# Performance work log

Hardware: AMD Instinct MI355X
Metric: run time of the kernel (lower is better)

Reference implementation:

```python
import jax, jax.numpy as jnp
import numpy as np

N_NODES = 50000
N_EDGES = 800000
IN_DIM = 64
HEADS = 8
DHEAD = 8
CLAMP = 5.0


def _xavier(key, shape, fan_in, fan_out):
    std = jnp.sqrt(2.0 / (fan_in + fan_out))
    return std * jax.random.normal(key, shape, dtype=jnp.float32)


def setup_inputs() -> dict:
    key = jax.random.key(0)
    ks = jax.random.split(key, 12)
    HD = HEADS * DHEAD
    x = jax.random.normal(ks[0], (N_NODES, IN_DIM), dtype=jnp.float32)
    edge_attr = jax.random.normal(ks[1], (N_EDGES, IN_DIM), dtype=jnp.float32)
    edge_index = jax.random.randint(ks[2], (2, N_EDGES), 0, N_NODES, dtype=jnp.int32)
    # Linear weights stored as [in, out] so y = x @ W + b
    WQ = _xavier(ks[3], (IN_DIM, HD), IN_DIM, HD)
    bQ = jnp.zeros((HD,), jnp.float32)
    WK = _xavier(ks[4], (IN_DIM, HD), IN_DIM, HD)
    bK = jnp.zeros((HD,), jnp.float32)
    WE = _xavier(ks[5], (IN_DIM, 2 * HD), IN_DIM, 2 * HD)
    bE = jnp.zeros((2 * HD,), jnp.float32)
    WV = _xavier(ks[6], (IN_DIM, HD), IN_DIM, HD)
    bV = jnp.zeros((HD,), jnp.float32)
    Aw = _xavier(ks[7], (DHEAD, HEADS, 1), DHEAD * HEADS, 1)
    VeRow = _xavier(ks[8], (DHEAD, HEADS, DHEAD), DHEAD * HEADS, DHEAD)
    return {"x": x, "edge_attr": edge_attr, "edge_index": edge_index,
            "WQ": WQ, "bQ": bQ, "WK": WK, "bK": bK, "WE": WE, "bE": bE,
            "WV": WV, "bV": bV, "Aw": Aw, "VeRow": VeRow}


def _forward(x, edge_attr, edge_index, WQ, bQ, WK, bK, WE, bE, WV, bV, Aw, VeRow):
    N = x.shape[0]
    src_idx = edge_index[0]
    dst_idx = edge_index[1]
    Q_h = (x @ WQ + bQ).reshape(N, HEADS, DHEAD)
    K_h = (x @ WK + bK).reshape(N, HEADS, DHEAD)
    V_h = (x @ WV + bV).reshape(N, HEADS, DHEAD)
    E = (edge_attr @ WE + bE).reshape(-1, HEADS, 2 * DHEAD)  # [E,H,2D]
    E_w, E_b = E[:, :, :DHEAD], E[:, :, DHEAD:]
    # per-edge score: gather + signed-sqrt transform
    score = K_h[src_idx] + Q_h[dst_idx]              # [E,H,D]
    score = score * E_w
    score = jnp.sqrt(jax.nn.relu(score)) - jnp.sqrt(jax.nn.relu(-score))
    score = score + E_b                               # act = Identity
    e_t = score
    wE = score.reshape(score.shape[0], HEADS * DHEAD)
    # attention logits: contract over head dim with Aw -> [E,H,1]
    logit = jnp.einsum('ehd,dhc->ehc', score, Aw)
    logit = jnp.clip(logit, -CLAMP, CLAMP)
    # segment softmax over destination nodes (pyg_softmax)
    smax = jax.ops.segment_max(logit, dst_idx, num_segments=N)
    ex = jnp.exp(logit - smax[dst_idx])
    denom = jax.ops.segment_sum(ex, dst_idx, num_segments=N)[dst_idx] + 1e-16
    attn = ex / denom                                 # [E,H,1], dropout p=0
    # message passing: scatter-add weighted values
    msg = V_h[src_idx] * attn                         # [E,H,D]
    wV = jax.ops.segment_sum(msg, dst_idx, num_segments=N)
    # edge enhancement
    rowV = jax.ops.segment_sum(e_t * attn, dst_idx, num_segments=N)  # [N,H,D]
    wV = wV + jnp.einsum('nhd,dhc->nhc', rowV, VeRow)
    return wV, wE


def reference(x, edge_attr, edge_index, WQ, bQ, WK, bK, WE, bE, WV, bV, Aw, VeRow):
    return _forward(x, edge_attr, edge_index, WQ, bQ, WK, bK, WE, bE, WV, bV, Aw, VeRow)
```

## Files before the change

### kernel.cpp

```cpp
#include <hip/hip_runtime.h>
#include <hip/hip_bf16.h>
#include <math.h>

#define N_NODES 50000
#define N_EDGES 800000
#define CLAMP_V 5.0f

typedef short short8 __attribute__((ext_vector_type(8)));
typedef float f32x4  __attribute__((ext_vector_type(4)));

static __device__ inline short f2bf(float x) {
    __hip_bfloat16 h = __float2bfloat16(x);
    return __builtin_bit_cast(short, h);
}
static __device__ inline float bf2f(short s) {
    unsigned u = ((unsigned)(unsigned short)s) << 16;
    return __builtin_bit_cast(float, u);
}

__global__ __launch_bounds__(256) void qkv_kernel(
    const float* __restrict__ x,
    const float* __restrict__ WQ, const float* __restrict__ bQ,
    const float* __restrict__ WK, const float* __restrict__ bK,
    const float* __restrict__ WV, const float* __restrict__ bV,
    float* __restrict__ Q, float* __restrict__ K, float* __restrict__ V)
{
    const int t = threadIdx.x;
    const int c = t & 63;
    const int nl = t >> 6;
    const int base = blockIdx.x * 16;

    float accQ[4], accK[4], accV[4];
    int nodes[4];
#pragma unroll
    for (int j = 0; j < 4; ++j) {
        nodes[j] = base + j * 4 + nl;
        accQ[j] = bQ[c]; accK[j] = bK[c]; accV[j] = bV[c];
    }
    for (int k = 0; k < 64; ++k) {
        const float wq = WQ[k * 64 + c];
        const float wk = WK[k * 64 + c];
        const float wv = WV[k * 64 + c];
#pragma unroll
        for (int j = 0; j < 4; ++j) {
            const float xv = x[nodes[j] * 64 + k];
            accQ[j] += xv * wq;
            accK[j] += xv * wk;
            accV[j] += xv * wv;
        }
    }
#pragma unroll
    for (int j = 0; j < 4; ++j) {
        const int n = nodes[j];
        Q[n * 64 + c] = accQ[j];
        K[n * 64 + c] = accK[j];
        V[n * 64 + c] = accV[j];
    }
}

__global__ __launch_bounds__(256, 3) void edge_kernel(
    const float* __restrict__ edge_attr,
    const int* __restrict__ src_idx, const int* __restrict__ dst_idx,
    const float* __restrict__ WE, const float* __restrict__ bE,
    const float* __restrict__ Aw,
    const float* __restrict__ Qn, const float* __restrict__ Kn,
    const float* __restrict__ Vn, const float* __restrict__ VeRow,
    float* __restrict__ wE_out, float* __restrict__ denom,
    float* __restrict__ wV_num)
{
    __shared__ __align__(16) char raw[41984];
    __shared__ float bEs[128];

    short8* Bhi = (short8*)raw;
    short8* Blo = (short8*)(raw + 16384);

    const int t = threadIdx.x;
    const int wave = t >> 6;
    const int lane = t & 63;

    short* BhiE = (short*)raw;
    short* BloE = (short*)(raw + 16384);
    for (int i = t; i < 8192; i += 256) {
        const int j  = i & 7;
        const int ln = (i >> 3) & 63;
        const int kh = (i >> 9) & 1;
        const int ct = i >> 10;
        const int k   = kh * 32 + ((ln >> 4) << 3) + j;
        const int col = (ct << 4) + (ln & 15);
        const float w = WE[k * 128 + col];
        const short hb = f2bf(w);
        BhiE[i] = hb;
        BloE[i] = f2bf(w - bf2f(hb));
    }
    if (t < 128) bEs[t] = bE[t];
    __syncthreads();

    float* Ebuf_w = (float*)(raw + 32768 + wave * 2304);

    const int h    = lane >> 3;
    const int kk   = lane & 7;
    const int g    = lane >> 4;
    const int c4   = lane & 15;
    const int h16k = (h << 4) + kk;
    const int ewoff = (h16k + (h16k >> 3)) << 2;
    const int eboff = ((h16k + 8) + ((h16k + 8) >> 3)) << 2;

    const float aw = Aw[kk * 8 + h];
    float veR[8];
#pragma unroll
    for (int dd = 0; dd < 8; ++dd) veR[dd] = VeRow[dd * 64 + lane];

    const int G = (int)gridDim.x;

    float4 arC[4], arN[4];
    int seC[16], deC[16], seN[16], deN[16];

    int it = blockIdx.x;
    {
        const int ebase0 = __builtin_amdgcn_readfirstlane(it * 64 + wave * 16);
#pragma unroll
        for (int p = 0; p < 2; ++p) {
            const float* srcp = edge_attr + (size_t)(ebase0 + c4) * 64 + p * 32 + (g << 3);
            arC[2 * p]     = *(const float4*)srcp;
            arC[2 * p + 1] = *(const float4*)(srcp + 4);
        }
#pragma unroll
        for (int r = 0; r < 16; ++r) {
            seC[r] = src_idx[ebase0 + r];
            deC[r] = dst_idx[ebase0 + r];
        }
    }

    for (; it < 12500; it += G) {
        const int ebaseC = __builtin_amdgcn_readfirstlane(it * 64 + wave * 16);
        const int itN    = it + G;
        const int itNc   = (itN < 12500) ? itN : 0;
        const int ebaseN = __builtin_amdgcn_readfirstlane(itNc * 64 + wave * 16);

        short8 ah[2], al[2];
#pragma unroll
        for (int p = 0; p < 2; ++p) {
            const float xv[8] = {arC[2*p].x, arC[2*p].y, arC[2*p].z, arC[2*p].w,
                                 arC[2*p+1].x, arC[2*p+1].y, arC[2*p+1].z, arC[2*p+1].w};
#pragma unroll
            for (int j = 0; j < 8; ++j) {
                const short hb = f2bf(xv[j]);
                ah[p][j] = hb;
                al[p][j] = f2bf(xv[j] - bf2f(hb));
            }
        }

#pragma unroll
        for (int r = 0; r < 16; ++r) {
            seN[r] = src_idx[ebaseN + r];
            deN[r] = dst_idx[ebaseN + r];
        }

        float vv[16], kv[16], qv[16];
#pragma unroll
        for (int r = 0; r < 16; ++r) vv[r] = Vn[seC[r] * 64 + lane];
#pragma unroll
        for (int r = 0; r < 16; ++r) {
            kv[r] = Kn[seC[r] * 64 + lane];
            qv[r] = Qn[deC[r] * 64 + lane];
        }

#pragma unroll
        for (int p = 0; p < 2; ++p) {
            const float* srcp = edge_attr + (size_t)(ebaseN + c4) * 64 + p * 32 + (g << 3);
            arN[2 * p]     = *(const float4*)srcp;
            arN[2 * p + 1] = *(const float4*)(srcp + 4);
        }

        f32x4 acc[8] = {};
        __builtin_amdgcn_s_setprio(1);
#pragma unroll
        for (int kh = 0; kh < 2; ++kh) {
#pragma unroll
            for (int ct = 0; ct < 8; ++ct) {
                const short8 bh = Bhi[(ct * 2 + kh) * 64 + lane];
                const short8 bl = Blo[(ct * 2 + kh) * 64 + lane];
                acc[ct] = __builtin_amdgcn_mfma_f32_16x16x32_bf16(ah[kh], bh, acc[ct], 0, 0, 0);
                acc[ct] = __builtin_amdgcn_mfma_f32_16x16x32_bf16(al[kh], bh, acc[ct], 0, 0, 0);
                acc[ct] = __builtin_amdgcn_mfma_f32_16x16x32_bf16(ah[kh], bl, acc[ct], 0, 0, 0);
            }
        }
        __builtin_amdgcn_s_setprio(0);

#pragma unroll
        for (int q = 0; q < 4; ++q) {
            if (g == q) {
#pragma unroll
                for (int ct = 0; ct < 8; ++ct) {
                    const int col = (ct << 4) + c4;
                    const float b = bEs[col];
                    f32x4 vq = acc[ct];
                    vq[0] += b; vq[1] += b; vq[2] += b; vq[3] += b;
                    *(f32x4*)(Ebuf_w + ((col + (col >> 3)) << 2)) = vq;
                }
            }
            __asm__ volatile("s_waitcnt lgkmcnt(0)" ::: "memory");
            __builtin_amdgcn_sched_barrier(0);
#pragma unroll
            for (int rr = 0; rr < 4; ++rr) {
                const int e = ebaseC + q * 4 + rr;
                const int d = deC[q * 4 + rr];
                const float kq = kv[q * 4 + rr] + qv[q * 4 + rr];
                const float ew = Ebuf_w[ewoff + rr];
                const float eb = Ebuf_w[eboff + rr];
                float sc = kq * ew;
                sc = copysignf(sqrtf(fabsf(sc)), sc) + eb;
                wE_out[(size_t)e * 64 + lane] = sc;

                float pp = sc * aw;
                pp += __shfl_xor(pp, 1);
                pp += __shfl_xor(pp, 2);
                pp += __shfl_xor(pp, 4);
                pp = fminf(fmaxf(pp, -CLAMP_V), CLAMP_V);
                const float ex = __expf(pp);
                if (kk == 0) unsafeAtomicAdd(&denom[d * 8 + h], ex);

                float rsum = 0.f;
#pragma unroll
                for (int dd = 0; dd < 8; ++dd) {
                    const float etd = __shfl(sc, (lane & 56) + dd);
                    rsum += etd * veR[dd];
                }
                unsafeAtomicAdd(&wV_num[(size_t)d * 64 + lane],
                                ex * (vv[q * 4 + rr] + rsum));
            }
            __builtin_amdgcn_sched_barrier(0);
        }

#pragma unroll
        for (int p = 0; p < 4; ++p) arC[p] = arN[p];
#pragma unroll
        for (int r = 0; r < 16; ++r) { seC[r] = seN[r]; deC[r] = deN[r]; }
    }
}

__global__ __launch_bounds__(256) void finalize_kernel(
    const float* __restrict__ denom, float* __restrict__ wV)
{
    const int i = blockIdx.x * 256 + threadIdx.x;
    const int n = i >> 6;
    const int h = (i >> 3) & 7;
    const float dn = denom[n * 8 + h] + 1e-16f;
    wV[i] = wV[i] / dn;
}

extern "C" void kernel_launch(void* const* d_in, const int* in_sizes, int n_in,
                              void* d_out, int out_size, void* d_ws, size_t ws_size,
                              hipStream_t stream) {
    const float* x         = (const float*)d_in[0];
    const float* edge_attr = (const float*)d_in[1];
    const int*   ei        = (const int*)  d_in[2];
    const float* WQ = (const float*)d_in[3];
    const float* bQ = (const float*)d_in[4];
    const float* WK = (const float*)d_in[5];
    const float* bK = (const float*)d_in[6];
    const float* WE = (const float*)d_in[7];
    const float* bE = (const float*)d_in[8];
    const float* WV = (const float*)d_in[9];
    const float* bV = (const float*)d_in[10];
    const float* Aw = (const float*)d_in[11];
    const float* VeRow = (const float*)d_in[12];

    float* out    = (float*)d_out;
    float* wV_out = out;
    float* wE_out = out + (size_t)N_NODES * 64;

    float* ws    = (float*)d_ws;
    float* Q     = ws;
    float* K     = ws + 3200000;
    float* V     = ws + 6400000;
    float* denom = ws + 9600000;

    const int* src_idx = ei;
    const int* dst_idx = ei + N_EDGES;

    hipMemsetAsync(wV_out, 0, (size_t)N_NODES * 64 * sizeof(float), stream);
    hipMemsetAsync(denom, 0, (size_t)N_NODES * 8 * sizeof(float), stream);

    qkv_kernel<<<3125, 256, 0, stream>>>(x, WQ, bQ, WK, bK, WV, bV, Q, K, V);
    edge_kernel<<<768, 256, 0, stream>>>(edge_attr, src_idx, dst_idx, WE, bE, Aw,
                                         Q, K, V, VeRow, wE_out, denom, wV_out);
    finalize_kernel<<<12500, 256, 0, stream>>>(denom, wV_out);
}
```

Baseline: 322.7 us.

## Sort edges by destination via counting sort and coalesce scatter atomics per run

Adds a histogram, single-block scan and scatter pass that build a destination-sorted permutation of edges each call. The edge kernel walks edges in permuted order and accumulates consecutive same-destination contributions in registers, issuing atomics only when the destination changes. This is meant to cut the number of global atomics to wV and denom and improve their locality. In exchange, edge_attr rows and wE writes become scattered, there are three extra launches including a serial single-block scan, and an extra indirection on perm.

```diff
diff --git a/kernel.cpp b/kernel.cpp
--- a/kernel.cpp
+++ b/kernel.cpp
@@ -58,9 +58,55 @@
     }
 }
 
+__global__ __launch_bounds__(256) void hist_kernel(
+    const int* __restrict__ dst_idx, int* __restrict__ cnt)
+{
+    const int e = blockIdx.x * 256 + threadIdx.x;
+    atomicAdd(&cnt[dst_idx[e]], 1);
+}
+
+__global__ __launch_bounds__(1024) void scan_kernel(int* __restrict__ cnt)
+{
+    __shared__ int ps[1024];
+    const int t = threadIdx.x;
+    const int base = t * 49;
+    int s = 0;
+    for (int i = 0; i < 49; ++i) {
+        const int idx = base + i;
+        s += (idx < N_NODES) ? cnt[idx] : 0;
+    }
+    ps[t] = s;
+    __syncthreads();
+    for (int d = 1; d < 1024; d <<= 1) {
+        int v = 0;
+        if (t >= d) v = ps[t - d];
+        __syncthreads();
+        ps[t] += v;
+        __syncthreads();
+    }
+    int run = ps[t] - s;
+    for (int i = 0; i < 49; ++i) {
+        const int idx = base + i;
+        if (idx < N_NODES) {
+            const int c = cnt[idx];
+            cnt[idx] = run;
+            run += c;
+        }
+    }
+}
+
+__global__ __launch_bounds__(256) void scatter_perm_kernel(
+    const int* __restrict__ dst_idx, int* __restrict__ cur, int* __restrict__ perm)
+{
+    const int e = blockIdx.x * 256 + threadIdx.x;
+    const int pos = atomicAdd(&cur[dst_idx[e]], 1);
+    perm[pos] = e;
+}
+
 __global__ __launch_bounds__(256, 3) void edge_kernel(
     const float* __restrict__ edge_attr,
     const int* __restrict__ src_idx, const int* __restrict__ dst_idx,
+    const int* __restrict__ perm,
     const float* __restrict__ WE, const float* __restrict__ bE,
     const float* __restrict__ Aw,
     const float* __restrict__ Qn, const float* __restrict__ Kn,
@@ -113,26 +159,28 @@
     const int G = (int)gridDim.x;
 
     float4 arC[4], arN[4];
-    int seC[16], deC[16], seN[16], deN[16];
+    int pmC[16], pmN[16], seC[16], deC[16], seN[16], deN[16];
 
     int it = blockIdx.x;
     {
         const int ebase0 = __builtin_amdgcn_readfirstlane(it * 64 + wave * 16);
 #pragma unroll
+        for (int r = 0; r < 16; ++r) pmC[r] = perm[ebase0 + r];
+#pragma unroll
+        for (int r = 0; r < 16; ++r) {
+            seC[r] = src_idx[pmC[r]];
+            deC[r] = dst_idx[pmC[r]];
+        }
+        const int vrow0 = perm[ebase0 + c4];
+#pragma unroll
         for (int p = 0; p < 2; ++p) {
-            const float* srcp = edge_attr + (size_t)(ebase0 + c4) * 64 + p * 32 + (g << 3);
+            const float* srcp = edge_attr + (size_t)vrow0 * 64 + p * 32 + (g << 3);
             arC[2 * p]     = *(const float4*)srcp;
             arC[2 * p + 1] = *(const float4*)(srcp + 4);
         }
-#pragma unroll
-        for (int r = 0; r < 16; ++r) {
-            seC[r] = src_idx[ebase0 + r];
-            deC[r] = dst_idx[ebase0 + r];
-        }
     }
 
     for (; it < 12500; it += G) {
-        const int ebaseC = __builtin_amdgcn_readfirstlane(it * 64 + wave * 16);
         const int itN    = it + G;
         const int itNc   = (itN < 12500) ? itN : 0;
         const int ebaseN = __builtin_amdgcn_readfirstlane(itNc * 64 + wave * 16);
@@ -151,9 +199,11 @@
         }
 
 #pragma unroll
+        for (int r = 0; r < 16; ++r) pmN[r] = perm[ebaseN + r];
+#pragma unroll
         for (int r = 0; r < 16; ++r) {
-            seN[r] = src_idx[ebaseN + r];
-            deN[r] = dst_idx[ebaseN + r];
+            seN[r] = src_idx[pmN[r]];
+            deN[r] = dst_idx[pmN[r]];
         }
 
         float vv[16], kv[16], qv[16];
@@ -165,11 +215,14 @@
             qv[r] = Qn[deC[r] * 64 + lane];
         }
 
-#pragma unroll
-        for (int p = 0; p < 2; ++p) {
-            const float* srcp = edge_attr + (size_t)(ebaseN + c4) * 64 + p * 32 + (g << 3);
-            arN[2 * p]     = *(const float4*)srcp;
-            arN[2 * p + 1] = *(const float4*)(srcp + 4);
+        {
+            const int vrowN = perm[ebaseN + c4];
+#pragma unroll
+            for (int p = 0; p < 2; ++p) {
+                const float* srcp = edge_attr + (size_t)vrowN * 64 + p * 32 + (g << 3);
+                arN[2 * p]     = *(const float4*)srcp;
+                arN[2 * p + 1] = *(const float4*)(srcp + 4);
+            }
         }
 
         f32x4 acc[8] = {};
@@ -187,6 +240,9 @@
         }
         __builtin_amdgcn_s_setprio(0);
 
+        int   runD  = -1;
+        float wvAcc = 0.f;
+        float dnAcc = 0.f;
 #pragma unroll
         for (int q = 0; q < 4; ++q) {
             if (g == q) {
@@ -203,7 +259,7 @@
             __builtin_amdgcn_sched_barrier(0);
 #pragma unroll
             for (int rr = 0; rr < 4; ++rr) {
-                const int e = ebaseC + q * 4 + rr;
+                const int e = pmC[q * 4 + rr];
                 const int d = deC[q * 4 + rr];
                 const float kq = kv[q * 4 + rr] + qv[q * 4 + rr];
                 const float ew = Ebuf_w[ewoff + rr];
@@ -218,7 +274,6 @@
                 pp += __shfl_xor(pp, 4);
                 pp = fminf(fmaxf(pp, -CLAMP_V), CLAMP_V);
                 const float ex = __expf(pp);
-                if (kk == 0) unsafeAtomicAdd(&denom[d * 8 + h], ex);
 
                 float rsum = 0.f;
 #pragma unroll
@@ -226,16 +281,27 @@
                     const float etd = __shfl(sc, (lane & 56) + dd);
                     rsum += etd * veR[dd];
                 }
-                unsafeAtomicAdd(&wV_num[(size_t)d * 64 + lane],
-                                ex * (vv[q * 4 + rr] + rsum));
+                const float contrib = ex * (vv[q * 4 + rr] + rsum);
+
+                if (d != runD) {
+                    if (runD >= 0) {
+                        unsafeAtomicAdd(&wV_num[(size_t)runD * 64 + lane], wvAcc);
+                        if (kk == 0) unsafeAtomicAdd(&denom[runD * 8 + h], dnAcc);
+                    }
+                    runD = d; wvAcc = 0.f; dnAcc = 0.f;
+                }
+                wvAcc += contrib;
+                dnAcc += ex;
             }
             __builtin_amdgcn_sched_barrier(0);
         }
+        unsafeAtomicAdd(&wV_num[(size_t)runD * 64 + lane], wvAcc);
+        if (kk == 0) unsafeAtomicAdd(&denom[runD * 8 + h], dnAcc);
 
 #pragma unroll
         for (int p = 0; p < 4; ++p) arC[p] = arN[p];
 #pragma unroll
-        for (int r = 0; r < 16; ++r) { seC[r] = seN[r]; deC[r] = deN[r]; }
+        for (int r = 0; r < 16; ++r) { pmC[r] = pmN[r]; seC[r] = seN[r]; deC[r] = deN[r]; }
     }
 }
 
@@ -275,15 +341,23 @@
     float* K     = ws + 3200000;
     float* V     = ws + 6400000;
     float* denom = ws + 9600000;
+    int*   cnt   = (int*)(ws + 10000000);
+    int*   perm  = (int*)(ws + 10050000);
 
     const int* src_idx = ei;
     const int* dst_idx = ei + N_EDGES;
 
     hipMemsetAsync(wV_out, 0, (size_t)N_NODES * 64 * sizeof(float), stream);
     hipMemsetAsync(denom, 0, (size_t)N_NODES * 8 * sizeof(float), stream);
+    hipMemsetAsync(cnt, 0, (size_t)N_NODES * sizeof(int), stream);
+
+    hist_kernel<<<3125, 256, 0, stream>>>(dst_idx, cnt);
+    scan_kernel<<<1, 1024, 0, stream>>>(cnt);
+    scatter_perm_kernel<<<3125, 256, 0, stream>>>(dst_idx, cnt, perm);
 
     qkv_kernel<<<3125, 256, 0, stream>>>(x, WQ, bQ, WK, bK, WV, bV, Q, K, V);
-    edge_kernel<<<768, 256, 0, stream>>>(edge_attr, src_idx, dst_idx, WE, bE, Aw,
-                                         Q, K, V, VeRow, wE_out, denom, wV_out);
+    edge_kernel<<<768, 256, 0, stream>>>(edge_attr, src_idx, dst_idx, perm,
+                                         WE, bE, Aw, Q, K, V, VeRow,
+                                         wE_out, denom, wV_out);
     finalize_kernel<<<12500, 256, 0, stream>>>(denom, wV_out);
 }
```

Result: slower. 488.4 us (+51.3%).

## Precompute WE bf16 fragments in a separate kernel and load from global

Applied to the files above, without the earlier changes.

Moves the hi/lo bf16 split of WE into a small pre-kernel that writes the fragments to workspace. The edge kernel now reloads them from global (L2-cached) into registers on every iteration instead of holding them in shared memory. This shrinks LDS from about 42 KB to about 9 KB per block and doubles the grid to 1536 blocks, aiming for more resident waves and less per-block setup. The risk is heavy VGPR pressure from 32 short8 fragments per lane, which could cause spills under the 3-blocks launch bound, plus repeated global or L2 traffic for the weights on each iteration.

```diff
diff --git a/kernel.cpp b/kernel.cpp
--- a/kernel.cpp
+++ b/kernel.cpp
@@ -58,44 +58,44 @@
     }
 }
 
+__global__ __launch_bounds__(256) void bfrag_kernel(
+    const float* __restrict__ WE, short* __restrict__ Bhig, short* __restrict__ Blog)
+{
+    const int i = blockIdx.x * 256 + threadIdx.x;
+    const int j  = i & 7;
+    const int ln = (i >> 3) & 63;
+    const int kh = (i >> 9) & 1;
+    const int ct = i >> 10;
+    const int k   = kh * 32 + ((ln >> 4) << 3) + j;
+    const int col = (ct << 4) + (ln & 15);
+    const float w = WE[k * 128 + col];
+    const short hb = f2bf(w);
+    Bhig[i] = hb;
+    Blog[i] = f2bf(w - bf2f(hb));
+}
+
 __global__ __launch_bounds__(256, 3) void edge_kernel(
     const float* __restrict__ edge_attr,
     const int* __restrict__ src_idx, const int* __restrict__ dst_idx,
-    const float* __restrict__ WE, const float* __restrict__ bE,
+    const short* __restrict__ Bhig, const short* __restrict__ Blog,
+    const float* __restrict__ bE,
     const float* __restrict__ Aw,
     const float* __restrict__ Qn, const float* __restrict__ Kn,
     const float* __restrict__ Vn, const float* __restrict__ VeRow,
     float* __restrict__ wE_out, float* __restrict__ denom,
     float* __restrict__ wV_num)
 {
-    __shared__ __align__(16) char raw[41984];
+    __shared__ __align__(16) char raw[9216];
     __shared__ float bEs[128];
-
-    short8* Bhi = (short8*)raw;
-    short8* Blo = (short8*)(raw + 16384);
 
     const int t = threadIdx.x;
     const int wave = t >> 6;
     const int lane = t & 63;
 
-    short* BhiE = (short*)raw;
-    short* BloE = (short*)(raw + 16384);
-    for (int i = t; i < 8192; i += 256) {
-        const int j  = i & 7;
-        const int ln = (i >> 3) & 63;
-        const int kh = (i >> 9) & 1;
-        const int ct = i >> 10;
-        const int k   = kh * 32 + ((ln >> 4) << 3) + j;
-        const int col = (ct << 4) + (ln & 15);
-        const float w = WE[k * 128 + col];
-        const short hb = f2bf(w);
-        BhiE[i] = hb;
-        BloE[i] = f2bf(w - bf2f(hb));
-    }
     if (t < 128) bEs[t] = bE[t];
     __syncthreads();
 
-    float* Ebuf_w = (float*)(raw + 32768 + wave * 2304);
+    float* Ebuf_w = (float*)(raw + wave * 2304);
 
     const int h    = lane >> 3;
     const int kk   = lane & 7;
@@ -110,6 +110,9 @@
 #pragma unroll
     for (int dd = 0; dd < 8; ++dd) veR[dd] = VeRow[dd * 64 + lane];
 
+    const short8* BhiG = (const short8*)Bhig;
+    const short8* BloG = (const short8*)Blog;
+
     const int G = (int)gridDim.x;
 
     float4 arC[4], arN[4];
@@ -137,6 +140,13 @@
         const int itNc   = (itN < 12500) ? itN : 0;
         const int ebaseN = __builtin_amdgcn_readfirstlane(itNc * 64 + wave * 16);
 
+        short8 bh[16], bl[16];
+#pragma unroll
+        for (int i = 0; i < 16; ++i) {
+            bh[i] = BhiG[i * 64 + lane];
+            bl[i] = BloG[i * 64 + lane];
+        }
+
         short8 ah[2], al[2];
 #pragma unroll
         for (int p = 0; p < 2; ++p) {
@@ -178,11 +188,11 @@
         for (int kh = 0; kh < 2; ++kh) {
 #pragma unroll
             for (int ct = 0; ct < 8; ++ct) {
-                const short8 bh = Bhi[(ct * 2 + kh) * 64 + lane];
-                const short8 bl = Blo[(ct * 2 + kh) * 64 + lane];
-                acc[ct] = __builtin_amdgcn_mfma_f32_16x16x32_bf16(ah[kh], bh, acc[ct], 0, 0, 0);
-                acc[ct] = __builtin_amdgcn_mfma_f32_16x16x32_bf16(al[kh], bh, acc[ct], 0, 0, 0);
-                acc[ct] = __builtin_amdgcn_mfma_f32_16x16x32_bf16(ah[kh], bl, acc[ct], 0, 0, 0);
+                const short8 bhv = bh[ct * 2 + kh];
+                const short8 blv = bl[ct * 2 + kh];
+                acc[ct] = __builtin_amdgcn_mfma_f32_16x16x32_bf16(ah[kh], bhv, acc[ct], 0, 0, 0);
+                acc[ct] = __builtin_amdgcn_mfma_f32_16x16x32_bf16(al[kh], bhv, acc[ct], 0, 0, 0);
+                acc[ct] = __builtin_amdgcn_mfma_f32_16x16x32_bf16(ah[kh], blv, acc[ct], 0, 0, 0);
             }
         }
         __builtin_amdgcn_s_setprio(0);
@@ -275,6 +285,8 @@
     float* K     = ws + 3200000;
     float* V     = ws + 6400000;
     float* denom = ws + 9600000;
+    short* Bhig  = (short*)(ws + 10000000);
+    short* Blog  = Bhig + 8192;
 
     const int* src_idx = ei;
     const int* dst_idx = ei + N_EDGES;
@@ -282,8 +294,10 @@
     hipMemsetAsync(wV_out, 0, (size_t)N_NODES * 64 * sizeof(float), stream);
     hipMemsetAsync(denom, 0, (size_t)N_NODES * 8 * sizeof(float), stream);
 
+    bfrag_kernel<<<32, 256, 0, stream>>>(WE, Bhig, Blog);
     qkv_kernel<<<3125, 256, 0, stream>>>(x, WQ, bQ, WK, bK, WV, bV, Q, K, V);
-    edge_kernel<<<768, 256, 0, stream>>>(edge_attr, src_idx, dst_idx, WE, bE, Aw,
-                                         Q, K, V, VeRow, wE_out, denom, wV_out);
+    edge_kernel<<<1536, 256, 0, stream>>>(edge_attr, src_idx, dst_idx, Bhig, Blog,
+                                          bE, Aw, Q, K, V, VeRow,
+                                          wE_out, denom, wV_out);
     finalize_kernel<<<12500, 256, 0, stream>>>(denom, wV_out);
 }
```

New measurement: 627.8 us. 1.95x slower.

## Defer VeRow projection to finalize by accumulating rowV numerators separately

Applied to the files above, without the earlier changes.

When workspace is large enough, the edge kernel no longer applies the per-edge VeRow contraction (8 shuffles and FMAs per edge). It instead atomically accumulates ex*score into a separate rowV buffer, and the finalize kernel applies VeRow once per node. This moves the contraction from per-edge to per-node work, but doubles the float atomics per edge and adds a memset and extra reads. The fold path runs only if ws_size covers the extra buffer.

```diff
diff --git a/kernel.cpp b/kernel.cpp
--- a/kernel.cpp
+++ b/kernel.cpp
@@ -58,6 +58,7 @@
     }
 }
 
+template<int FOLD_VE>
 __global__ __launch_bounds__(256, 3) void edge_kernel(
     const float* __restrict__ edge_attr,
     const int* __restrict__ src_idx, const int* __restrict__ dst_idx,
@@ -66,7 +67,7 @@
     const float* __restrict__ Qn, const float* __restrict__ Kn,
     const float* __restrict__ Vn, const float* __restrict__ VeRow,
     float* __restrict__ wE_out, float* __restrict__ denom,
-    float* __restrict__ wV_num)
+    float* __restrict__ wV_num, float* __restrict__ rowV_num)
 {
     __shared__ __align__(16) char raw[41984];
     __shared__ float bEs[128];
@@ -107,8 +108,10 @@
 
     const float aw = Aw[kk * 8 + h];
     float veR[8];
-#pragma unroll
-    for (int dd = 0; dd < 8; ++dd) veR[dd] = VeRow[dd * 64 + lane];
+    if (!FOLD_VE) {
+#pragma unroll
+        for (int dd = 0; dd < 8; ++dd) veR[dd] = VeRow[dd * 64 + lane];
+    }
 
     const int G = (int)gridDim.x;
 
@@ -220,14 +223,19 @@
                 const float ex = __expf(pp);
                 if (kk == 0) unsafeAtomicAdd(&denom[d * 8 + h], ex);
 
-                float rsum = 0.f;
-#pragma unroll
-                for (int dd = 0; dd < 8; ++dd) {
-                    const float etd = __shfl(sc, (lane & 56) + dd);
-                    rsum += etd * veR[dd];
+                if (FOLD_VE) {
+                    unsafeAtomicAdd(&wV_num[(size_t)d * 64 + lane], ex * vv[q * 4 + rr]);
+                    unsafeAtomicAdd(&rowV_num[(size_t)d * 64 + lane], ex * sc);
+                } else {
+                    float rsum = 0.f;
+#pragma unroll
+                    for (int dd = 0; dd < 8; ++dd) {
+                        const float etd = __shfl(sc, (lane & 56) + dd);
+                        rsum += etd * veR[dd];
+                    }
+                    unsafeAtomicAdd(&wV_num[(size_t)d * 64 + lane],
+                                    ex * (vv[q * 4 + rr] + rsum));
                 }
-                unsafeAtomicAdd(&wV_num[(size_t)d * 64 + lane],
-                                ex * (vv[q * 4 + rr] + rsum));
             }
             __builtin_amdgcn_sched_barrier(0);
         }
@@ -239,14 +247,30 @@
     }
 }
 
+template<int FOLD_VE>
 __global__ __launch_bounds__(256) void finalize_kernel(
-    const float* __restrict__ denom, float* __restrict__ wV)
+    const float* __restrict__ denom, const float* __restrict__ rowV_num,
+    const float* __restrict__ VeRow, float* __restrict__ wV)
 {
-    const int i = blockIdx.x * 256 + threadIdx.x;
+    __shared__ float VeL[512];
+    const int t = threadIdx.x;
+    if (FOLD_VE) {
+        for (int i = t; i < 512; i += 256) VeL[i] = VeRow[i];
+        __syncthreads();
+    }
+    const int i = blockIdx.x * 256 + t;
     const int n = i >> 6;
-    const int h = (i >> 3) & 7;
+    const int lane6 = i & 63;
+    const int h = lane6 >> 3;
     const float dn = denom[n * 8 + h] + 1e-16f;
-    wV[i] = wV[i] / dn;
+    float num = wV[i];
+    if (FOLD_VE) {
+#pragma unroll
+        for (int dd = 0; dd < 8; ++dd) {
+            num += rowV_num[n * 64 + h * 8 + dd] * VeL[dd * 64 + lane6];
+        }
+    }
+    wV[i] = num / dn;
 }
 
 extern "C" void kernel_launch(void* const* d_in, const int* in_sizes, int n_in,
@@ -275,15 +299,25 @@
     float* K     = ws + 3200000;
     float* V     = ws + 6400000;
     float* denom = ws + 9600000;
+    float* rowV  = ws + 10000000;
+
+    const bool fold = (ws_size >= (size_t)13200000 * sizeof(float));
 
     const int* src_idx = ei;
     const int* dst_idx = ei + N_EDGES;
 
     hipMemsetAsync(wV_out, 0, (size_t)N_NODES * 64 * sizeof(float), stream);
     hipMemsetAsync(denom, 0, (size_t)N_NODES * 8 * sizeof(float), stream);
+    if (fold) hipMemsetAsync(rowV, 0, (size_t)N_NODES * 64 * sizeof(float), stream);
 
     qkv_kernel<<<3125, 256, 0, stream>>>(x, WQ, bQ, WK, bK, WV, bV, Q, K, V);
-    edge_kernel<<<768, 256, 0, stream>>>(edge_attr, src_idx, dst_idx, WE, bE, Aw,
-                                         Q, K, V, VeRow, wE_out, denom, wV_out);
-    finalize_kernel<<<12500, 256, 0, stream>>>(denom, wV_out);
-}
+    if (fold) {
+        edge_kernel<1><<<768, 256, 0, stream>>>(edge_attr, src_idx, dst_idx, WE, bE, Aw,
+                                                Q, K, V, VeRow, wE_out, denom, wV_out, rowV);
+        finalize_kernel<1><<<12500, 256, 0, stream>>>(denom, rowV, VeRow, wV_out);
+    } else {
+        edge_kernel<0><<<768, 256, 0, stream>>>(edge_attr, src_idx, dst_idx, WE, bE, Aw,
+                                                Q, K, V, VeRow, wE_out, denom, wV_out, rowV);
+        finalize_kernel<0><<<12500, 256, 0, stream>>>(denom, rowV, VeRow, wV_out);
+    }
+}
```

Result: slower. 483.4 us (+49.8%).
